# Kernel optimization log

Measured on AMD Instinct MI355X. Metric: run time of the kernel, lower is better.

## Reference

```python
import jax, jax.numpy as jnp
import numpy as np

WINDOW = 3
SEQ_LEN = 41
FEATURE = 128
FILTER_NUM = 128
PAD = WINDOW // 2


def setup_inputs() -> dict:
    key = jax.random.key(0)
    k1, k2 = jax.random.split(key)
    B = 4096
    inputs = jax.random.normal(k1, (B, SEQ_LEN, FEATURE), dtype=jnp.float32)
    # per-position Linear weights: 41 independent [window*feature -> filter_num] layers
    fan_in = WINDOW * FEATURE
    W = jax.random.normal(k2, (SEQ_LEN, fan_in, FILTER_NUM), dtype=jnp.float32) / np.sqrt(fan_in)
    b = jnp.zeros((SEQ_LEN, FILTER_NUM), dtype=jnp.float32)
    return {"inputs": inputs, "W": W, "b": b}


def reference(inputs, W, b):
    # inputs: [B, S, F]; pad sequence dim by PAD zeros on each side
    xpad = jnp.pad(inputs, ((0, 0), (PAD, PAD), (0, 0)))  # [B, S+2*PAD, F]
    # gather windows: idx[s, w] = s + w -> [B, S, WINDOW, F]
    idx = jnp.arange(SEQ_LEN)[:, None] + jnp.arange(WINDOW)[None, :]
    xw = xpad[:, idx, :]
    B = inputs.shape[0]
    xw = xw.reshape(B, SEQ_LEN, WINDOW * FEATURE)  # [B, S, W*F]
    # per-position linear (locally-connected): one batched GEMM over positions
    out = jnp.einsum('bsd,sdf->bsf', xw, W) + b[None, :, :]
    # ReLU; Dropout(0.5) is identity in eval mode
    return jax.nn.relu(out)
```

## Files before the change

kernel.cpp:

```cpp
#include <hip/hip_runtime.h>

#define SEQ 41
#define FEAT 128
#define KDIM 384
#define ROWLEN (SEQ * FEAT)
#define BM 256

typedef float floatx4 __attribute__((ext_vector_type(4)));
typedef __bf16 bf16x8 __attribute__((ext_vector_type(8)));
typedef unsigned short ushortx8 __attribute__((ext_vector_type(8)));

__device__ __forceinline__ unsigned short f2bf(float f) {
    unsigned int u = __builtin_bit_cast(unsigned int, f);
    return (unsigned short)((u + 0x7fffu + ((u >> 16) & 1u)) >> 16);
}

__device__ __forceinline__ bf16x8 pack8(floatx4 lo, floatx4 hi) {
    bf16x8 r;
#pragma unroll
    for (int j = 0; j < 4; j++) { r[j] = (__bf16)lo[j]; r[4 + j] = (__bf16)hi[j]; }
    return r;
}

#define DMA16(g, l)                                                          \
    __builtin_amdgcn_global_load_lds(                                        \
        (const __attribute__((address_space(1))) void*)(g),                  \
        (__attribute__((address_space(3))) void*)(l), 16, 0, 0)

__global__ __launch_bounds__(256) void wt2_kernel(const float* __restrict__ W,
                                                  unsigned short* __restrict__ Wt2) {
    int t = blockIdx.x * 256 + threadIdx.x;
    int s = t / 6144, g = t % 6144;
    int lane = g & 63, nt = (g >> 6) & 7, ks = (g >> 9) & 1, slab = g >> 10;
    int n  = nt * 16 + (lane & 15);
    int k0 = slab * 64 + ks * 32 + (lane >> 4) * 8;
    const float* Ws = W + (size_t)s * KDIM * FEAT;
    ushortx8 v;
#pragma unroll
    for (int j = 0; j < 8; j++) v[j] = f2bf(Ws[(size_t)(k0 + j) * FEAT + n]);
    *reinterpret_cast<ushortx8*>(Wt2 + (size_t)t * 8) = v;
}

template <int USE_WT>
__global__ __launch_bounds__(512, 2) void gemm_kernel(const float* __restrict__ X,
                                                      const void* __restrict__ Wsrc,
                                                      const float* __restrict__ bias,
                                                      float* __restrict__ out) {
    __shared__ unsigned short Bs[6 * 8192];

    const int tid  = threadIdx.x;
    const int lane = tid & 63;
    const int wv   = tid >> 6;
    const int s    = blockIdx.y;
    const int m0   = blockIdx.x * BM + wv * 32;

    const int klo = (s == 0) ? 2 : 0;
    const int khi = (s == SEQ - 1) ? 4 : 6;
    const int nk  = khi - klo;
    const int nst = nk * 2;

    const int colq = lane & 15, quad = lane >> 4;

    const int koff = (s - 1) * FEAT + klo * 64 + quad * 8;
    const float* aptr0 = X + (size_t)(m0 + colq) * ROWLEN + koff;
    const float* aptr1 = aptr0 + (size_t)16 * ROWLEN;

    floatx4 acc[2][8];
#pragma unroll
    for (int mi = 0; mi < 2; mi++)
#pragma unroll
        for (int ni = 0; ni < 8; ni++) acc[mi][ni] = (floatx4){0.f, 0.f, 0.f, 0.f};

    struct Abuf { floatx4 L0, H0, L1, H1; };
    Abuf A0, A1, A2, A3;

    auto loadA = [&](Abuf& ab, int ksi) {
        const float* p0 = aptr0 + ksi * 32;
        const float* p1 = aptr1 + ksi * 32;
        ab.L0 = *reinterpret_cast<const floatx4*>(p0);
        ab.H0 = *reinterpret_cast<const floatx4*>(p0 + 4);
        ab.L1 = *reinterpret_cast<const floatx4*>(p1);
        ab.H1 = *reinterpret_cast<const floatx4*>(p1 + 4);
    };

    auto step = [&](const Abuf& ab, int ksi) {
        bf16x8 bfr[8];
        const unsigned short* bp = &Bs[ksi * 4096 + lane * 8];
#pragma unroll
        for (int ni = 0; ni < 8; ni++)
            bfr[ni] = *reinterpret_cast<const bf16x8*>(bp + ni * 512);
        bf16x8 af0 = pack8(ab.L0, ab.H0);
        bf16x8 af1 = pack8(ab.L1, ab.H1);
        __builtin_amdgcn_s_setprio(1);
#pragma unroll
        for (int ni = 0; ni < 8; ni++) {
            acc[0][ni] = __builtin_amdgcn_mfma_f32_16x16x32_bf16(af0, bfr[ni], acc[0][ni], 0, 0, 0);
            acc[1][ni] = __builtin_amdgcn_mfma_f32_16x16x32_bf16(af1, bfr[ni], acc[1][ni], 0, 0, 0);
        }
        __builtin_amdgcn_s_setprio(0);
    };

    loadA(A0, 0); loadA(A1, 1); loadA(A2, 2); loadA(A3, 3);

    if (USE_WT) {
        const unsigned short* wsrc =
            (const unsigned short*)Wsrc + ((size_t)s * 6 + klo) * 8192;
        const int nwi = nk * 16;
        for (int i = wv; i < nwi; i += 8)
            DMA16(wsrc + (size_t)i * 512 + lane * 8, &Bs[(size_t)i * 512]);
    } else {
        const float* Wf = (const float*)Wsrc;
        for (int j = tid; j < nk * 1024; j += 512) {
            int ln = j & 63, nt = (j >> 6) & 7, ksa = j >> 9;
            int k = klo * 64 + ksa * 32 + (ln >> 4) * 8;
            int n = nt * 16 + (ln & 15);
            ushortx8 v;
#pragma unroll
            for (int jj = 0; jj < 8; jj++)
                v[jj] = f2bf(Wf[((size_t)s * KDIM + k + jj) * FEAT + n]);
            *reinterpret_cast<ushortx8*>(&Bs[(size_t)j * 8]) = v;
        }
    }
    __syncthreads();

    int ksi = 0;
    for (; ksi + 4 < nst; ksi += 4) {
        step(A0, ksi + 0); loadA(A0, ksi + 4);
        step(A1, ksi + 1); loadA(A1, ksi + 5);
        step(A2, ksi + 2); loadA(A2, ksi + 6);
        step(A3, ksi + 3); loadA(A3, ksi + 7);
    }
    step(A0, ksi + 0); step(A1, ksi + 1); step(A2, ksi + 2); step(A3, ksi + 3);

#pragma unroll
    for (int ni = 0; ni < 8; ni++) {
        int n = ni * 16 + colq;
        float bv = bias[s * FEAT + n];
#pragma unroll
        for (int mi = 0; mi < 2; mi++) {
            size_t base = ((size_t)(m0 + mi * 16 + quad * 4) * SEQ + s) * FEAT + n;
#pragma unroll
            for (int r = 0; r < 4; r++) {
                float v = acc[mi][ni][r] + bv;
                v = v > 0.f ? v : 0.f;
                out[base + (size_t)r * (SEQ * FEAT)] = v;
            }
        }
    }
}

extern "C" void kernel_launch(void* const* d_in, const int* in_sizes, int n_in,
                              void* d_out, int out_size, void* d_ws, size_t ws_size,
                              hipStream_t stream) {
    const float* X    = (const float*)d_in[0];
    const float* W    = (const float*)d_in[1];
    const float* bias = (const float*)d_in[2];
    float* out = (float*)d_out;

    const int B = in_sizes[0] / ROWLEN;
    dim3 grid(B / BM, SEQ);

    const size_t wt_bytes = (size_t)SEQ * 6 * 8192 * sizeof(unsigned short);
    if (ws_size >= wt_bytes) {
        unsigned short* Wt2 = (unsigned short*)d_ws;
        wt2_kernel<<<(SEQ * 6144) / 256, 256, 0, stream>>>(W, Wt2);
        gemm_kernel<1><<<grid, 512, 0, stream>>>(X, (const void*)Wt2, bias, out);
    } else {
        gemm_kernel<0><<<grid, 512, 0, stream>>>(X, (const void*)W, bias, out);
    }
}
```

Measured before the change: 192.1 us.

## Remap blocks across XCDs for L2 locality and issue A prefetch earlier

The 2D grid becomes a 1D grid whose block index is remapped so that each XCD handles a contiguous set of batch panels and runs neighbouring sequence positions close together in time. Overlapping input windows (s-1, s, s+1) should then hit the same XCD's L2. The A-tile prefetch for ksi+4 is also issued right after converting the current registers to bf16, behind a sched_barrier, so global loads go out before the LDS reads and MFMAs. The remap assumes eight XCDs with round-robin dispatch and 41 positions grouped in sevens, and falls back to a plain mapping otherwise.

```diff
diff --git a/kernel.cpp b/kernel.cpp
--- a/kernel.cpp
+++ b/kernel.cpp
@@ -48,11 +48,26 @@
                                                       float* __restrict__ out) {
     __shared__ unsigned short Bs[6 * 8192];
 
+    const int nbx = (int)gridDim.x / SEQ;
+    int panel, s;
+    if ((nbx & 7) == 0) {
+        const int npx  = nbx >> 3;
+        const int xcd  = (int)blockIdx.x & 7;
+        const int k    = (int)blockIdx.x >> 3;
+        const int full = 7 * npx;
+        int c = k / full;
+        int j = k - c * full;
+        int q = j / npx;
+        s     = c * 7 + q;
+        panel = xcd * npx + (j - q * npx);
+    } else {
+        panel = (int)blockIdx.x % nbx; s = (int)blockIdx.x / nbx;
+    }
+
     const int tid  = threadIdx.x;
     const int lane = tid & 63;
     const int wv   = tid >> 6;
-    const int s    = blockIdx.y;
-    const int m0   = blockIdx.x * BM + wv * 32;
+    const int m0   = panel * BM + wv * 32;
 
     const int klo = (s == 0) ? 2 : 0;
     const int khi = (s == SEQ - 1) ? 4 : 6;
@@ -83,14 +98,16 @@
         ab.H1 = *reinterpret_cast<const floatx4*>(p1 + 4);
     };
 
-    auto step = [&](const Abuf& ab, int ksi) {
+    auto step = [&](Abuf& ab, int ksi, bool pf) {
+        bf16x8 af0 = pack8(ab.L0, ab.H0);
+        bf16x8 af1 = pack8(ab.L1, ab.H1);
+        if (pf) loadA(ab, ksi + 4);
+        __builtin_amdgcn_sched_barrier(0);
+        const unsigned short* bp = &Bs[ksi * 4096 + lane * 8];
         bf16x8 bfr[8];
-        const unsigned short* bp = &Bs[ksi * 4096 + lane * 8];
 #pragma unroll
         for (int ni = 0; ni < 8; ni++)
             bfr[ni] = *reinterpret_cast<const bf16x8*>(bp + ni * 512);
-        bf16x8 af0 = pack8(ab.L0, ab.H0);
-        bf16x8 af1 = pack8(ab.L1, ab.H1);
         __builtin_amdgcn_s_setprio(1);
 #pragma unroll
         for (int ni = 0; ni < 8; ni++) {
@@ -125,12 +142,13 @@
 
     int ksi = 0;
     for (; ksi + 4 < nst; ksi += 4) {
-        step(A0, ksi + 0); loadA(A0, ksi + 4);
-        step(A1, ksi + 1); loadA(A1, ksi + 5);
-        step(A2, ksi + 2); loadA(A2, ksi + 6);
-        step(A3, ksi + 3); loadA(A3, ksi + 7);
+        step(A0, ksi + 0, true);
+        step(A1, ksi + 1, true);
+        step(A2, ksi + 2, true);
+        step(A3, ksi + 3, true);
     }
-    step(A0, ksi + 0); step(A1, ksi + 1); step(A2, ksi + 2); step(A3, ksi + 3);
+    step(A0, ksi + 0, false); step(A1, ksi + 1, false);
+    step(A2, ksi + 2, false); step(A3, ksi + 3, false);
 
 #pragma unroll
     for (int ni = 0; ni < 8; ni++) {
@@ -158,7 +176,8 @@
     float* out = (float*)d_out;
 
     const int B = in_sizes[0] / ROWLEN;
-    dim3 grid(B / BM, SEQ);
+    const int nbx = B / BM;
+    dim3 grid(nbx * SEQ);
 
     const size_t wt_bytes = (size_t)SEQ * 6 * 8192 * sizeof(unsigned short);
     if (ws_size >= wt_bytes) {
```

Result: no change. 190.8 us (-0.7%).
